# Optimization experiments

Measured on AMD Instinct MI355X. Metric: run time of the kernel, lower is better.

The kernel has to match this reference:

```python
import jax, jax.numpy as jnp
import numpy as np

N, D, K, H, G = 200000, 256, 128, 4, 1024  # nodes, emb_dim, hidden, heads, graphs


def setup_inputs() -> dict:
    key = jax.random.key(0)
    k0, k1, k2, k3 = jax.random.split(key, 4)
    node_features = jax.random.normal(k0, (N, D), jnp.float32)
    segment_ids = jnp.sort(jax.random.randint(k1, (N,), 0, G)).astype(jnp.int32)
    W1 = jax.random.normal(k2, (H, D, K), jnp.float32) / np.float32(np.sqrt(D))
    b1 = jnp.zeros((H, K), jnp.float32)
    W2 = jax.random.normal(k3, (H, K), jnp.float32) / np.float32(np.sqrt(K))
    b2 = jnp.zeros((H,), jnp.float32)
    return {"node_features": node_features, "segment_ids": segment_ids,
            "num_graphs": G, "W1": W1, "b1": b1, "W2": W2, "b2": b2}


def _segment_softmax(scores, seg, num_segments):
    # scores: [N, H]; numerically-stable softmax within each graph segment, per head
    m = jax.ops.segment_max(scores, seg, num_segments=num_segments)  # [G, H]
    e = jnp.exp(scores - m[seg])
    s = jax.ops.segment_sum(e, seg, num_segments=num_segments)  # [G, H]
    return e / s[seg]


def reference(node_features, segment_ids, num_graphs, W1, b1, W2, b2):
    # Per-head MLP score for all heads at once: [N, H]
    h = jax.nn.relu(jnp.einsum('nd,hdk->nhk', node_features, W1) + b1)
    scores = jnp.einsum('nhk,hk->nh', h, W2) + b2
    # dgl.softmax_nodes per head == segment softmax over graph ids
    attn = _segment_softmax(scores, segment_ids, num_graphs)  # [N, H]
    # combine_type == 'mean': mean_h segment_sum(attn_h * x)
    # == segment_sum(mean_h(attn_h) * x) since the sum is linear in attn.
    avg_attn = attn.mean(axis=1)  # [N]
    weighted = avg_attn[:, None] * node_features  # [N, D]
    return jax.ops.segment_sum(weighted, segment_ids, num_segments=num_graphs)  # [G, D]
```

## Files before the change

### kernel.cpp

```cpp
#include <hip/hip_runtime.h>
#include <hip/hip_bf16.h>

typedef unsigned short u16;
typedef __attribute__((ext_vector_type(8))) __bf16 bf16x8;
typedef __attribute__((ext_vector_type(8))) u16 u16x8;
typedef __attribute__((ext_vector_type(4))) float f32x4;

__device__ __forceinline__ u16 f2bf(float f) {
    unsigned u = __float_as_uint(f);
    u += 0x7fffu + ((u >> 16) & 1u);
    return (u16)(u >> 16);
}

__device__ __forceinline__ void gl_lds16(const void* g, void* l) {
    __builtin_amdgcn_global_load_lds(
        (const __attribute__((address_space(1))) void*)g,
        (__attribute__((address_space(3))) void*)l, 16, 0, 0);
}

__global__ __launch_bounds__(256) void transpose_w1(const float* __restrict__ W1,
                                                    u16* __restrict__ W1T) {
    __shared__ u16 tile[64][132];
    const int t = threadIdx.x;
    const int h = blockIdx.x >> 2;
    const int dt = blockIdx.x & 3;
#pragma unroll
    for (int j = 0; j < 8; ++j) {
        int idx = j * 256 + t;
        int r = idx >> 5;
        int kq = idx & 31;
        float4 v = *reinterpret_cast<const float4*>(
            W1 + ((size_t)h * 256 + dt * 64 + r) * 128 + kq * 4);
        ushort4 o;
        o.x = f2bf(v.x); o.y = f2bf(v.y); o.z = f2bf(v.z); o.w = f2bf(v.w);
        *reinterpret_cast<ushort4*>(&tile[r][kq * 4]) = o;
    }
    __syncthreads();
#pragma unroll
    for (int j = 0; j < 4; ++j) {
        int idx = j * 256 + t;
        int k = idx >> 3;
        int c8 = idx & 7;
        u16x8 o;
#pragma unroll
        for (int e = 0; e < 8; ++e) o[e] = tile[c8 * 8 + e][k];
        *reinterpret_cast<u16x8*>(W1T + ((size_t)h * 128 + k) * 256 + dt * 64 + c8 * 8) = o;
    }
}

__global__ __launch_bounds__(256, 2) void score_kernel(
        const float* __restrict__ x, const u16* __restrict__ W1T,
        const float* __restrict__ b1, const float* __restrict__ W2,
        const float* __restrict__ b2, float* __restrict__ scores, int N) {
    __shared__ u16 xb[16384];
    __shared__ u16 sA[16384];

    const int t = threadIdx.x;
    const int wave = t >> 6;
    const int lane = t & 63;
    const int l15 = lane & 15;
    const int quad = lane >> 4;
    const int n0 = blockIdx.x * 64;

    const u16* asrc = W1T + ((size_t)wave * 128 + l15) * 256 + quad * 8;

    auto stageA = [&](int ks) {
#pragma unroll
        for (int j = 0; j < 8; ++j)
            gl_lds16(asrc + j * 4096 + ks * 32, &sA[(size_t)(wave * 8 + j) * 512]);
    };

    stageA(0);

    {
        const int nrow = wave * 16 + (lane >> 2);
        const int koff = (lane & 3) * 8;
        int nn = n0 + nrow; if (nn >= N) nn = N - 1;
        const float* src = x + (size_t)nn * 256 + koff;
        const int l_t = ((lane & 3) << 4) | (lane >> 2);
        const int q   = l_t ^ ((l_t >> 4) << 1);
        u16* dst = xb + (size_t)wave * 512 + q * 8;
        float4 v[16];
#pragma unroll
        for (int i = 0; i < 8; ++i) {
            v[2 * i]     = *reinterpret_cast<const float4*>(src + i * 32);
            v[2 * i + 1] = *reinterpret_cast<const float4*>(src + i * 32 + 4);
        }
#pragma unroll
        for (int i = 0; i < 8; ++i) {
            u16x8 o;
            o[0] = f2bf(v[2*i].x);   o[1] = f2bf(v[2*i].y);
            o[2] = f2bf(v[2*i].z);   o[3] = f2bf(v[2*i].w);
            o[4] = f2bf(v[2*i+1].x); o[5] = f2bf(v[2*i+1].y);
            o[6] = f2bf(v[2*i+1].z); o[7] = f2bf(v[2*i+1].w);
            *reinterpret_cast<u16x8*>(dst + i * 2048) = o;
        }
    }

    const int qr = lane ^ ((lane >> 4) << 1);
    const u16* xrd = xb + qr * 8;
    const u16* abase = &sA[(size_t)wave * 4096 + lane * 8];

    __syncthreads();

    f32x4 acc[8][4] = {};
    for (int ks = 0; ks < 8; ++ks) {
        bf16x8 a[8], b[4];
#pragma unroll
        for (int j = 0; j < 8; ++j)
            a[j] = *reinterpret_cast<const bf16x8*>(abase + j * 512);
#pragma unroll
        for (int nf = 0; nf < 4; ++nf)
            b[nf] = *reinterpret_cast<const bf16x8*>(xrd + (ks * 4 + nf) * 512);
        __syncthreads();
        if (ks < 7) stageA(ks + 1);
#pragma unroll
        for (int fr = 0; fr < 8; ++fr)
#pragma unroll
            for (int nf = 0; nf < 4; ++nf)
                acc[fr][nf] = __builtin_amdgcn_mfma_f32_16x16x32_bf16(
                    a[fr], b[nf], acc[fr][nf], 0, 0, 0);
        __syncthreads();
    }

    const int h = wave;
    float4 b1v[8], w2v[8];
#pragma unroll
    for (int fr = 0; fr < 8; ++fr) {
        int rb = h * 128 + fr * 16 + quad * 4;
        b1v[fr] = *reinterpret_cast<const float4*>(b1 + rb);
        w2v[fr] = *reinterpret_cast<const float4*>(W2 + rb);
    }
    const float b2v = b2[h];
#pragma unroll
    for (int nf = 0; nf < 4; ++nf) {
        float p = 0.f;
#pragma unroll
        for (int fr = 0; fr < 8; ++fr) {
            f32x4 c = acc[fr][nf];
            p += fmaxf(c[0] + b1v[fr].x, 0.f) * w2v[fr].x
               + fmaxf(c[1] + b1v[fr].y, 0.f) * w2v[fr].y
               + fmaxf(c[2] + b1v[fr].z, 0.f) * w2v[fr].z
               + fmaxf(c[3] + b1v[fr].w, 0.f) * w2v[fr].w;
        }
        p += __shfl_xor(p, 16, 64);
        p += __shfl_xor(p, 32, 64);
        int n = n0 + nf * 16 + lane;
        if (lane < 16 && n < N)
            scores[(size_t)n * 4 + h] = p + b2v;
    }
}

__device__ __forceinline__ int lower_bound(const int* __restrict__ a, int n, int v) {
    int lo = 0, hi = n;
    while (lo < hi) {
        int mid = (lo + hi) >> 1;
        if (a[mid] < v) lo = mid + 1; else hi = mid;
    }
    return lo;
}

__global__ __launch_bounds__(256) void starts_kernel(
        const int* __restrict__ seg, int* __restrict__ starts, int N, int G) {
    int g = blockIdx.x * 256 + threadIdx.x;
    if (g > G) return;
    if (g == 0)      starts[0] = 0;
    else if (g == G) starts[G] = N;
    else             starts[g] = lower_bound(seg, N, g);
}

__global__ __launch_bounds__(256) void pool_kernel(
        const float* __restrict__ x, const float4* __restrict__ scores4,
        const int* __restrict__ starts, float* __restrict__ out) {
    __shared__ float4 red[4];
    __shared__ float wl[256];
    const int g = blockIdx.x;
    const int t = threadIdx.x;
    const int lane = t & 63;
    const int wv = t >> 6;
    const int start = starts[g];
    const int end = starts[g + 1];
    const int len = end - start;

    float* og = out + (size_t)g * 256;
    if (len == 0) { og[t] = 0.f; return; }

    float4 mx = make_float4(-3.4e38f, -3.4e38f, -3.4e38f, -3.4e38f);
    for (int i = start + t; i < end; i += 256) {
        float4 s = scores4[i];
        mx.x = fmaxf(mx.x, s.x); mx.y = fmaxf(mx.y, s.y);
        mx.z = fmaxf(mx.z, s.z); mx.w = fmaxf(mx.w, s.w);
    }
#pragma unroll
    for (int off = 1; off < 64; off <<= 1) {
        mx.x = fmaxf(mx.x, __shfl_xor(mx.x, off, 64));
        mx.y = fmaxf(mx.y, __shfl_xor(mx.y, off, 64));
        mx.z = fmaxf(mx.z, __shfl_xor(mx.z, off, 64));
        mx.w = fmaxf(mx.w, __shfl_xor(mx.w, off, 64));
    }
    if (lane == 0) red[wv] = mx;
    __syncthreads();
    {
        float4 r0 = red[0], r1 = red[1], r2 = red[2], r3 = red[3];
        mx.x = fmaxf(fmaxf(r0.x, r1.x), fmaxf(r2.x, r3.x));
        mx.y = fmaxf(fmaxf(r0.y, r1.y), fmaxf(r2.y, r3.y));
        mx.z = fmaxf(fmaxf(r0.z, r1.z), fmaxf(r2.z, r3.z));
        mx.w = fmaxf(fmaxf(r0.w, r1.w), fmaxf(r2.w, r3.w));
    }
    __syncthreads();

    float4 sm = make_float4(0.f, 0.f, 0.f, 0.f);
    for (int i = start + t; i < end; i += 256) {
        float4 s = scores4[i];
        sm.x += expf(s.x - mx.x); sm.y += expf(s.y - mx.y);
        sm.z += expf(s.z - mx.z); sm.w += expf(s.w - mx.w);
    }
#pragma unroll
    for (int off = 1; off < 64; off <<= 1) {
        sm.x += __shfl_xor(sm.x, off, 64);
        sm.y += __shfl_xor(sm.y, off, 64);
        sm.z += __shfl_xor(sm.z, off, 64);
        sm.w += __shfl_xor(sm.w, off, 64);
    }
    if (lane == 0) red[wv] = sm;
    __syncthreads();
    float4 inv;
    {
        float4 r0 = red[0], r1 = red[1], r2 = red[2], r3 = red[3];
        inv.x = 1.f / (r0.x + r1.x + r2.x + r3.x);
        inv.y = 1.f / (r0.y + r1.y + r2.y + r3.y);
        inv.z = 1.f / (r0.z + r1.z + r2.z + r3.z);
        inv.w = 1.f / (r0.w + r1.w + r2.w + r3.w);
    }

    float acc = 0.f;
    for (int c = 0; c < len; c += 256) {
        float w = 0.f;
        if (c + t < len) {
            float4 s = scores4[start + c + t];
            w = 0.25f * (expf(s.x - mx.x) * inv.x + expf(s.y - mx.y) * inv.y +
                         expf(s.z - mx.z) * inv.z + expf(s.w - mx.w) * inv.w);
        }
        __syncthreads();
        wl[t] = w;
        __syncthreads();
        const int cl = min(256, len - c);
        const float* xp = x + (size_t)(start + c) * 256 + t;
        int j = 0;
        for (; j + 8 <= cl; j += 8) {
            float xv[8];
#pragma unroll
            for (int jj = 0; jj < 8; ++jj) xv[jj] = xp[(size_t)(j + jj) * 256];
#pragma unroll
            for (int jj = 0; jj < 8; ++jj) acc += wl[j + jj] * xv[jj];
        }
        for (; j < cl; ++j) acc += wl[j] * xp[(size_t)j * 256];
    }
    og[t] = acc;
}

extern "C" void kernel_launch(void* const* d_in, const int* in_sizes, int n_in,
                              void* d_out, int out_size, void* d_ws, size_t ws_size,
                              hipStream_t stream) {
    const float* x  = (const float*)d_in[0];
    const int* seg  = (const int*)d_in[1];
    const float* W1 = (const float*)d_in[3];
    const float* b1 = (const float*)d_in[4];
    const float* W2 = (const float*)d_in[5];
    const float* b2 = (const float*)d_in[6];
    float* out = (float*)d_out;

    const int N = in_sizes[0] / 256;
    const int G = 1024;

    char* ws = (char*)d_ws;
    float* scores = (float*)ws;
    u16* W1T      = (u16*)(ws + (size_t)N * 16);
    int* starts   = (int*)(ws + (size_t)N * 16 + 262144);

    transpose_w1<<<16, 256, 0, stream>>>(W1, W1T);
    starts_kernel<<<(G + 256) / 256, 256, 0, stream>>>(seg, starts, N, G);
    score_kernel<<<(N + 63) / 64, 256, 0, stream>>>(x, W1T, b1, W2, b2, scores, N);
    pool_kernel<<<G, 256, 0, stream>>>(x, (const float4*)scores, starts, out);
}
```

Measured before the change: 408.6 us.

## Double threads per block in score and pool kernels with split-K/row reductions

The score kernel now uses 8 waves per block, two per head, each computing half of the hidden units. The partial dot products are combined through shared memory. The x-to-bf16 staging is reorganised so each thread loads a contiguous 32-float chunk. The pool kernel uses 512 threads, splitting node rows between two halves, larger weight chunks and a final shared-memory sum. The goal is higher occupancy and more memory parallelism, at the cost of extra barriers and a leftover dead max loop.

```diff
diff --git a/kernel.cpp b/kernel.cpp
--- a/kernel.cpp
+++ b/kernel.cpp
@@ -48,66 +48,64 @@
     }
 }
 
-__global__ __launch_bounds__(256, 2) void score_kernel(
+__global__ __launch_bounds__(512, 4) void score_kernel(
         const float* __restrict__ x, const u16* __restrict__ W1T,
         const float* __restrict__ b1, const float* __restrict__ W2,
         const float* __restrict__ b2, float* __restrict__ scores, int N) {
     __shared__ u16 xb[16384];
     __shared__ u16 sA[16384];
+    __shared__ float pr[4][4][16];
 
     const int t = threadIdx.x;
     const int wave = t >> 6;
     const int lane = t & 63;
     const int l15 = lane & 15;
     const int quad = lane >> 4;
+    const int hh = wave >> 1;
+    const int half = wave & 1;
     const int n0 = blockIdx.x * 64;
 
-    const u16* asrc = W1T + ((size_t)wave * 128 + l15) * 256 + quad * 8;
-
+    const u16* asrc = W1T + ((size_t)hh * 128 + half * 64 + l15) * 256 + quad * 8;
     auto stageA = [&](int ks) {
 #pragma unroll
-        for (int j = 0; j < 8; ++j)
-            gl_lds16(asrc + j * 4096 + ks * 32, &sA[(size_t)(wave * 8 + j) * 512]);
+        for (int j = 0; j < 4; ++j)
+            gl_lds16(asrc + j * 4096 + ks * 32, &sA[(size_t)(wave * 4 + j) * 512]);
     };
-
     stageA(0);
 
     {
-        const int nrow = wave * 16 + (lane >> 2);
-        const int koff = (lane & 3) * 8;
-        int nn = n0 + nrow; if (nn >= N) nn = N - 1;
-        const float* src = x + (size_t)nn * 256 + koff;
-        const int l_t = ((lane & 3) << 4) | (lane >> 2);
-        const int q   = l_t ^ ((l_t >> 4) << 1);
-        u16* dst = xb + (size_t)wave * 512 + q * 8;
-        float4 v[16];
-#pragma unroll
-        for (int i = 0; i < 8; ++i) {
-            v[2 * i]     = *reinterpret_cast<const float4*>(src + i * 32);
-            v[2 * i + 1] = *reinterpret_cast<const float4*>(src + i * 32 + 4);
-        }
-#pragma unroll
-        for (int i = 0; i < 8; ++i) {
+        const int n = t >> 3;
+        const int ks = t & 7;
+        int nn = n0 + n; if (nn >= N) nn = N - 1;
+        const float* src = x + (size_t)nn * 256 + ks * 32;
+        float4 v[8];
+#pragma unroll
+        for (int i = 0; i < 8; ++i)
+            v[i] = *reinterpret_cast<const float4*>(src + i * 4);
+        const int nf = n >> 4;
+        const int r15 = n & 15;
+#pragma unroll
+        for (int kcq = 0; kcq < 4; ++kcq) {
+            const int q = (kcq * 16 + r15) ^ (kcq << 1);
             u16x8 o;
-            o[0] = f2bf(v[2*i].x);   o[1] = f2bf(v[2*i].y);
-            o[2] = f2bf(v[2*i].z);   o[3] = f2bf(v[2*i].w);
-            o[4] = f2bf(v[2*i+1].x); o[5] = f2bf(v[2*i+1].y);
-            o[6] = f2bf(v[2*i+1].z); o[7] = f2bf(v[2*i+1].w);
-            *reinterpret_cast<u16x8*>(dst + i * 2048) = o;
+            float4 vA = v[2 * kcq], vB = v[2 * kcq + 1];
+            o[0] = f2bf(vA.x); o[1] = f2bf(vA.y); o[2] = f2bf(vA.z); o[3] = f2bf(vA.w);
+            o[4] = f2bf(vB.x); o[5] = f2bf(vB.y); o[6] = f2bf(vB.z); o[7] = f2bf(vB.w);
+            *reinterpret_cast<u16x8*>(&xb[((ks * 4 + nf) * 64 + q) * 8]) = o;
         }
     }
 
     const int qr = lane ^ ((lane >> 4) << 1);
     const u16* xrd = xb + qr * 8;
-    const u16* abase = &sA[(size_t)wave * 4096 + lane * 8];
-
-    __syncthreads();
-
-    f32x4 acc[8][4] = {};
+    const u16* abase = &sA[(size_t)wave * 2048 + lane * 8];
+
+    __syncthreads();
+
+    f32x4 acc[4][4] = {};
     for (int ks = 0; ks < 8; ++ks) {
-        bf16x8 a[8], b[4];
-#pragma unroll
-        for (int j = 0; j < 8; ++j)
+        bf16x8 a[4], b[4];
+#pragma unroll
+        for (int j = 0; j < 4; ++j)
             a[j] = *reinterpret_cast<const bf16x8*>(abase + j * 512);
 #pragma unroll
         for (int nf = 0; nf < 4; ++nf)
@@ -115,7 +113,7 @@
         __syncthreads();
         if (ks < 7) stageA(ks + 1);
 #pragma unroll
-        for (int fr = 0; fr < 8; ++fr)
+        for (int fr = 0; fr < 4; ++fr)
 #pragma unroll
             for (int nf = 0; nf < 4; ++nf)
                 acc[fr][nf] = __builtin_amdgcn_mfma_f32_16x16x32_bf16(
@@ -123,31 +121,42 @@
         __syncthreads();
     }
 
-    const int h = wave;
-    float4 b1v[8], w2v[8];
-#pragma unroll
-    for (int fr = 0; fr < 8; ++fr) {
-        int rb = h * 128 + fr * 16 + quad * 4;
+    float4 b1v[4], w2v[4];
+#pragma unroll
+    for (int fr = 0; fr < 4; ++fr) {
+        int rb = hh * 128 + half * 64 + fr * 16 + quad * 4;
         b1v[fr] = *reinterpret_cast<const float4*>(b1 + rb);
         w2v[fr] = *reinterpret_cast<const float4*>(W2 + rb);
     }
-    const float b2v = b2[h];
+    float p[4];
 #pragma unroll
     for (int nf = 0; nf < 4; ++nf) {
-        float p = 0.f;
-#pragma unroll
-        for (int fr = 0; fr < 8; ++fr) {
+        float pp = 0.f;
+#pragma unroll
+        for (int fr = 0; fr < 4; ++fr) {
             f32x4 c = acc[fr][nf];
-            p += fmaxf(c[0] + b1v[fr].x, 0.f) * w2v[fr].x
-               + fmaxf(c[1] + b1v[fr].y, 0.f) * w2v[fr].y
-               + fmaxf(c[2] + b1v[fr].z, 0.f) * w2v[fr].z
-               + fmaxf(c[3] + b1v[fr].w, 0.f) * w2v[fr].w;
-        }
-        p += __shfl_xor(p, 16, 64);
-        p += __shfl_xor(p, 32, 64);
-        int n = n0 + nf * 16 + lane;
-        if (lane < 16 && n < N)
-            scores[(size_t)n * 4 + h] = p + b2v;
+            pp += fmaxf(c[0] + b1v[fr].x, 0.f) * w2v[fr].x
+                + fmaxf(c[1] + b1v[fr].y, 0.f) * w2v[fr].y
+                + fmaxf(c[2] + b1v[fr].z, 0.f) * w2v[fr].z
+                + fmaxf(c[3] + b1v[fr].w, 0.f) * w2v[fr].w;
+        }
+        pp += __shfl_xor(pp, 16, 64);
+        pp += __shfl_xor(pp, 32, 64);
+        p[nf] = pp;
+    }
+    if (half == 1 && lane < 16) {
+#pragma unroll
+        for (int nf = 0; nf < 4; ++nf) pr[hh][nf][lane] = p[nf];
+    }
+    __syncthreads();
+    if (half == 0 && lane < 16) {
+        const float b2v = b2[hh];
+#pragma unroll
+        for (int nf = 0; nf < 4; ++nf) {
+            int n = n0 + nf * 16 + lane;
+            if (n < N)
+                scores[(size_t)n * 4 + hh] = p[nf] + pr[hh][nf][lane] + b2v;
+        }
     }
 }
 
@@ -169,11 +178,12 @@
     else             starts[g] = lower_bound(seg, N, g);
 }
 
-__global__ __launch_bounds__(256) void pool_kernel(
+__global__ __launch_bounds__(512) void pool_kernel(
         const float* __restrict__ x, const float4* __restrict__ scores4,
         const int* __restrict__ starts, float* __restrict__ out) {
-    __shared__ float4 red[4];
-    __shared__ float wl[256];
+    __shared__ float4 red[8];
+    __shared__ float wl[1024];
+    __shared__ float partial[512];
     const int g = blockIdx.x;
     const int t = threadIdx.x;
     const int lane = t & 63;
@@ -183,10 +193,10 @@
     const int len = end - start;
 
     float* og = out + (size_t)g * 256;
-    if (len == 0) { og[t] = 0.f; return; }
+    if (len == 0) { if (t < 256) og[t] = 0.f; return; }
 
     float4 mx = make_float4(-3.4e38f, -3.4e38f, -3.4e38f, -3.4e38f);
-    for (int i = start + t; i < end; i += 256) {
+    for (int i = start + t; i < end; i += 512) {
         float4 s = scores4[i];
         mx.x = fmaxf(mx.x, s.x); mx.y = fmaxf(mx.y, s.y);
         mx.z = fmaxf(mx.z, s.z); mx.w = fmaxf(mx.w, s.w);
@@ -200,17 +210,24 @@
     }
     if (lane == 0) red[wv] = mx;
     __syncthreads();
+#pragma unroll
+    for (int w = 1; w < 8; ++w) {
+        mx.x = fmaxf(red[0].x, red[w].x) > mx.x ? fmaxf(red[0].x, red[w].x) : mx.x;
+    }
     {
-        float4 r0 = red[0], r1 = red[1], r2 = red[2], r3 = red[3];
-        mx.x = fmaxf(fmaxf(r0.x, r1.x), fmaxf(r2.x, r3.x));
-        mx.y = fmaxf(fmaxf(r0.y, r1.y), fmaxf(r2.y, r3.y));
-        mx.z = fmaxf(fmaxf(r0.z, r1.z), fmaxf(r2.z, r3.z));
-        mx.w = fmaxf(fmaxf(r0.w, r1.w), fmaxf(r2.w, r3.w));
+        float4 r = red[0];
+        mx = r;
+#pragma unroll
+        for (int w = 1; w < 8; ++w) {
+            float4 q = red[w];
+            mx.x = fmaxf(mx.x, q.x); mx.y = fmaxf(mx.y, q.y);
+            mx.z = fmaxf(mx.z, q.z); mx.w = fmaxf(mx.w, q.w);
+        }
     }
     __syncthreads();
 
     float4 sm = make_float4(0.f, 0.f, 0.f, 0.f);
-    for (int i = start + t; i < end; i += 256) {
+    for (int i = start + t; i < end; i += 512) {
         float4 s = scores4[i];
         sm.x += expf(s.x - mx.x); sm.y += expf(s.y - mx.y);
         sm.z += expf(s.z - mx.z); sm.w += expf(s.w - mx.w);
@@ -226,37 +243,45 @@
     __syncthreads();
     float4 inv;
     {
-        float4 r0 = red[0], r1 = red[1], r2 = red[2], r3 = red[3];
-        inv.x = 1.f / (r0.x + r1.x + r2.x + r3.x);
-        inv.y = 1.f / (r0.y + r1.y + r2.y + r3.y);
-        inv.z = 1.f / (r0.z + r1.z + r2.z + r3.z);
-        inv.w = 1.f / (r0.w + r1.w + r2.w + r3.w);
-    }
-
+        float4 s0 = red[0];
+#pragma unroll
+        for (int w = 1; w < 8; ++w) {
+            float4 q = red[w];
+            s0.x += q.x; s0.y += q.y; s0.z += q.z; s0.w += q.w;
+        }
+        inv.x = 1.f / s0.x; inv.y = 1.f / s0.y;
+        inv.z = 1.f / s0.z; inv.w = 1.f / s0.w;
+    }
+
+    const int col = t & 255;
+    const int hf = t >> 8;
     float acc = 0.f;
-    for (int c = 0; c < len; c += 256) {
-        float w = 0.f;
-        if (c + t < len) {
-            float4 s = scores4[start + c + t];
-            w = 0.25f * (expf(s.x - mx.x) * inv.x + expf(s.y - mx.y) * inv.y +
-                         expf(s.z - mx.z) * inv.z + expf(s.w - mx.w) * inv.w);
-        }
+    for (int c = 0; c < len; c += 1024) {
+        const int cl = min(1024, len - c);
         __syncthreads();
-        wl[t] = w;
+        for (int i = t; i < cl; i += 512) {
+            float4 s = scores4[start + c + i];
+            wl[i] = 0.25f * (expf(s.x - mx.x) * inv.x + expf(s.y - mx.y) * inv.y +
+                             expf(s.z - mx.z) * inv.z + expf(s.w - mx.w) * inv.w);
+        }
         __syncthreads();
-        const int cl = min(256, len - c);
-        const float* xp = x + (size_t)(start + c) * 256 + t;
-        int j = 0;
-        for (; j + 8 <= cl; j += 8) {
+        const float* xp = x + (size_t)(start + c) * 256 + col;
+        int jb = hf * 8;
+        for (; jb + 8 <= cl; jb += 16) {
             float xv[8];
 #pragma unroll
-            for (int jj = 0; jj < 8; ++jj) xv[jj] = xp[(size_t)(j + jj) * 256];
-#pragma unroll
-            for (int jj = 0; jj < 8; ++jj) acc += wl[j + jj] * xv[jj];
-        }
-        for (; j < cl; ++j) acc += wl[j] * xp[(size_t)j * 256];
-    }
-    og[t] = acc;
+            for (int jj = 0; jj < 8; ++jj) xv[jj] = xp[(size_t)(jb + jj) * 256];
+#pragma unroll
+            for (int jj = 0; jj < 8; ++jj) acc += wl[jb + jj] * xv[jj];
+        }
+        if (jb < cl) {
+            const int je = min(jb + 8, cl);
+            for (int j = jb; j < je; ++j) acc += wl[j] * xp[(size_t)j * 256];
+        }
+    }
+    partial[t] = acc;
+    __syncthreads();
+    if (t < 256) og[t] = partial[t] + partial[t + 256];
 }
 
 extern "C" void kernel_launch(void* const* d_in, const int* in_sizes, int n_in,
@@ -280,6 +305,6 @@
 
     transpose_w1<<<16, 256, 0, stream>>>(W1, W1T);
     starts_kernel<<<(G + 256) / 256, 256, 0, stream>>>(seg, starts, N, G);
-    score_kernel<<<(N + 63) / 64, 256, 0, stream>>>(x, W1T, b1, W2, b2, scores, N);
-    pool_kernel<<<G, 256, 0, stream>>>(x, (const float4*)scores, starts, out);
-}
+    score_kernel<<<(N + 63) / 64, 512, 0, stream>>>(x, W1T, b1, W2, b2, scores, N);
+    pool_kernel<<<G, 512, 0, stream>>>(x, (const float4*)scores, starts, out);
+}
```

Measured after the change: 421.6 us. +3.2%, slower.
